# Performance work log

Measured on AMD Instinct MI355X. Metric: run time of the kernel, lower is better.

## Reference

```python
import jax, jax.numpy as jnp
import numpy as np

D_MODEL = 1024
NUM_HEADS = 16
D_K = D_MODEL // NUM_HEADS
D_FF = 4096


def setup_inputs() -> dict:
    key = jax.random.key(0)
    ks = jax.random.split(key, 12)
    s = 1.0 / np.sqrt(D_MODEL)
    sf = 1.0 / np.sqrt(D_FF)
    return {
        "x": jax.random.normal(ks[0], (2, 2048, D_MODEL), dtype=jnp.float32),
        # nn.Linear weights are [out_features, in_features]
        "Wq": jax.random.uniform(ks[1], (D_MODEL, D_MODEL), jnp.float32, -s, s),
        "Wk": jax.random.uniform(ks[2], (D_MODEL, D_MODEL), jnp.float32, -s, s),
        "Wv": jax.random.uniform(ks[3], (D_MODEL, D_MODEL), jnp.float32, -s, s),
        "Wo": jax.random.uniform(ks[4], (D_MODEL, D_MODEL), jnp.float32, -s, s),
        "W1": jax.random.uniform(ks[5], (D_FF, D_MODEL), jnp.float32, -s, s),
        "W2": jax.random.uniform(ks[6], (D_MODEL, D_FF), jnp.float32, -sf, sf),
        "g1": jnp.ones((D_MODEL,), jnp.float32),
        "b1": jnp.zeros((D_MODEL,), jnp.float32),
        "g2": jnp.ones((D_MODEL,), jnp.float32),
        "b2": jnp.zeros((D_MODEL,), jnp.float32),
    }


def _layer_norm(x, gamma, beta, eps=1e-5):
    mu = jnp.mean(x, axis=-1, keepdims=True)
    var = jnp.mean((x - mu) ** 2, axis=-1, keepdims=True)
    return (x - mu) * jax.lax.rsqrt(var + eps) * gamma + beta


def reference(x, Wq, Wk, Wv, Wo, W1, W2, g1, b1, g2, b2):
    B, S, _ = x.shape
    H, Dk = NUM_HEADS, D_K
    # projections (Linear: x @ W.T), split heads -> [B, H, S, Dk]
    q = (x @ Wq.T).reshape(B, S, H, Dk).transpose(0, 2, 1, 3)
    k = (x @ Wk.T).reshape(B, S, H, Dk).transpose(0, 2, 1, 3)
    v = (x @ Wv.T).reshape(B, S, H, Dk).transpose(0, 2, 1, 3)
    scores = jnp.einsum('bhsd,bhtd->bhst', q, k) / jnp.sqrt(jnp.float32(Dk))
    attn = jax.nn.softmax(scores, axis=-1)
    out = jnp.einsum('bhst,bhtd->bhsd', attn, v)
    out = out.transpose(0, 2, 1, 3).reshape(B, S, H * Dk)
    out = out @ Wo.T
    x_after_attn = _layer_norm(x + out, g1, b1)
    ff = jax.nn.gelu(x_after_attn @ W1.T, approximate=False)
    ff_out = ff @ W2.T
    return _layer_norm(x_after_attn + ff_out, g2, b2)
```

## Files before the change

### kernel.cpp

```cpp
#include <hip/hip_runtime.h>
#include <hip/hip_bf16.h>
#include <cstdint>
#include <cstddef>

#define D_MODEL 1024
#define D_FF    4096
#define NTOK    4096
#define SEQ     2048
#define NH      16
#define DK      64
#define LDQ     3072

typedef __bf16 bf16;
typedef __bf16 bf16_8 __attribute__((ext_vector_type(8)));
typedef __bf16 bf16_4 __attribute__((ext_vector_type(4)));
typedef float  f32_4  __attribute__((ext_vector_type(4)));

__device__ __forceinline__ void async_copy16(const bf16* g, bf16* l) {
    __builtin_amdgcn_global_load_lds((const __attribute__((address_space(1))) void*)g,
                                     (__attribute__((address_space(3))) void*)l,
                                     16, 0, 0);
}

__global__ __launch_bounds__(256)
void cast_all(const float* __restrict__ x,  const float* __restrict__ Wq,
              const float* __restrict__ Wk, const float* __restrict__ Wv,
              const float* __restrict__ Wo, const float* __restrict__ W1,
              const float* __restrict__ W2,
              bf16* __restrict__ xb, bf16* __restrict__ Wqkvb,
              bf16* __restrict__ Wob, bf16* __restrict__ W1b,
              bf16* __restrict__ W2b) {
    const int blk = blockIdx.x;
    const float* s; bf16* d; int off;
    if (blk < 4096)       { s = x;  d = xb;              off = blk; }
    else if (blk < 5120)  { s = Wq; d = Wqkvb;           off = blk - 4096; }
    else if (blk < 6144)  { s = Wk; d = Wqkvb + 1048576; off = blk - 5120; }
    else if (blk < 7168)  { s = Wv; d = Wqkvb + 2097152; off = blk - 6144; }
    else if (blk < 8192)  { s = Wo; d = Wob;             off = blk - 7168; }
    else if (blk < 12288) { s = W1; d = W1b;             off = blk - 8192; }
    else                  { s = W2; d = W2b;             off = blk - 12288; }
    const int i = off * 1024 + threadIdx.x * 4;
    float4 v = *(const float4*)(s + i);
    bf16_4 o;
    o[0] = (bf16)v.x; o[1] = (bf16)v.y; o[2] = (bf16)v.z; o[3] = (bf16)v.w;
    *(bf16_4*)(d + i) = o;
}

template <int EPI>
__global__ __launch_bounds__(256, 2)
void gemm_bt(const bf16* __restrict__ A, const bf16* __restrict__ B,
             bf16* __restrict__ C0, bf16* __restrict__ C1,
             int M, int N, int ldk, int kLen) {
    __shared__ bf16 As[128 * 32];
    __shared__ bf16 Bs[128 * 32];
    const int tid  = threadIdx.x;
    const int wave = tid >> 6, lane = tid & 63;
    const int quad = lane >> 4, l15 = lane & 15;
    const int wm = wave >> 1, wn = wave & 1;
    const int bm = blockIdx.x, bn = blockIdx.y, z = blockIdx.z;

    const bf16* A0 = A + (size_t)bm * 128 * ldk + (size_t)z * kLen;
    const bf16* B0 = B + (size_t)bn * 128 * ldk + (size_t)z * kLen;

    f32_4 acc[4][4];
#pragma unroll
    for (int i = 0; i < 4; i++)
#pragma unroll
        for (int j = 0; j < 4; j++) acc[i][j] = (f32_4){0.f, 0.f, 0.f, 0.f};

    const int ra = tid >> 2;
    const int gl = (tid & 3) ^ ((ra >> 1) & 3);
    const int ca = gl * 8;
    const int sx = (l15 >> 1) & 3;

    for (int k0 = 0; k0 < kLen; k0 += 32) {
#pragma unroll
        for (int c = 0; c < 2; c++)
            async_copy16(&A0[(size_t)(c * 64 + ra) * ldk + k0 + ca],
                         &As[c * 2048 + wave * 512]);
#pragma unroll
        for (int c = 0; c < 2; c++)
            async_copy16(&B0[(size_t)(c * 64 + ra) * ldk + k0 + ca],
                         &Bs[c * 2048 + wave * 512]);
        __syncthreads();

        bf16_8 af[4], bfr[4];
#pragma unroll
        for (int mi = 0; mi < 4; mi++)
            af[mi] = *(const bf16_8*)&As[(wm * 64 + mi * 16 + l15) * 32 + ((quad ^ sx) * 8)];
#pragma unroll
        for (int ni = 0; ni < 4; ni++)
            bfr[ni] = *(const bf16_8*)&Bs[(wn * 64 + ni * 16 + l15) * 32 + ((quad ^ sx) * 8)];
#pragma unroll
        for (int mi = 0; mi < 4; mi++)
#pragma unroll
            for (int ni = 0; ni < 4; ni++)
                acc[mi][ni] = __builtin_amdgcn_mfma_f32_16x16x32_bf16(
                    af[mi], bfr[ni], acc[mi][ni], 0, 0, 0);
        __syncthreads();
    }

    bf16* C = z ? C1 : C0;
    const int row0 = bm * 128 + wm * 64 + quad * 4;
    const int col0 = bn * 128 + wn * 64 + l15;
#pragma unroll
    for (int mi = 0; mi < 4; mi++) {
#pragma unroll
        for (int ni = 0; ni < 4; ni++) {
#pragma unroll
            for (int r = 0; r < 4; r++) {
                int row = row0 + mi * 16 + r;
                int col = col0 + ni * 16;
                size_t idx = (size_t)row * N + col;
                float v = acc[mi][ni][r];
                if (EPI == 0) {
                    C[idx] = (bf16)v;
                } else {
                    float g = 0.5f * v * (1.0f + erff(v * 0.70710678118654752f));
                    C[idx] = (bf16)g;
                }
            }
        }
    }
}

__global__ __launch_bounds__(256)
void transpose_v(const bf16* __restrict__ QKV, bf16* __restrict__ Vt) {
    __shared__ bf16 T[64 * 72];
    const int tb = blockIdx.x;
    const int cb = blockIdx.y;
    const int tid = threadIdx.x;
    const int r = tid >> 3, g = tid & 7;
#pragma unroll
    for (int c = 0; c < 2; ++c) {
        int row = c * 32 + r;
        bf16_8 v = *(const bf16_8*)&QKV[(size_t)(tb * 64 + row) * LDQ + 2048 + cb * 64 + g * 8];
        *(bf16_8*)&T[row * 72 + g * 8] = v;
    }
    __syncthreads();
    const int b  = (tb * 64) >> 11;
    const int s0 = (tb * 64) & 2047;
#pragma unroll
    for (int c = 0; c < 2; ++c) {
        int ch = c * 32 + r;
        bf16_8 v;
#pragma unroll
        for (int j = 0; j < 8; ++j) v[j] = T[(g * 8 + j) * 72 + ch];
        *(bf16_8*)&Vt[(size_t)(b * 1024 + cb * 64 + ch) * SEQ + s0 + g * 8] = v;
    }
}

__global__ __launch_bounds__(256)
void attn3(const bf16* __restrict__ QKV, const bf16* __restrict__ Vt,
           bf16* __restrict__ O) {
    __shared__ bf16 Ks[64 * 64];
    __shared__ bf16 Vs[64 * 64];
    __shared__ bf16 Ps[4][16 * 80];

    const int tid  = threadIdx.x;
    const int wave = tid >> 6, lane = tid & 63;
    const int quad = lane >> 4, l15 = lane & 15;
    const int qb = blockIdx.x & 31;
    const int h  = (blockIdx.x >> 5) & 15;
    const int b  = blockIdx.x >> 9;

    const bf16* Qg = QKV + (size_t)(b * SEQ) * LDQ + h * 64;
    const bf16* Kg = QKV + (size_t)(b * SEQ) * LDQ + 1024 + h * 64;
    const bf16* Vg = Vt + (size_t)(b * 1024 + h * 64) * SEQ;

    const int qrow = qb * 64 + wave * 16 + l15;
    const bf16_8 qf0 = *(const bf16_8*)&Qg[(size_t)qrow * LDQ + quad * 8];
    const bf16_8 qf1 = *(const bf16_8*)&Qg[(size_t)qrow * LDQ + 32 + quad * 8];

    const int srow = wave * 8 + (lane >> 3);
    const int sg   = lane & 7;
    const int xl   = l15 & 7;

    float l_lane = 0.f;
    f32_4 o_acc[4];
#pragma unroll
    for (int d = 0; d < 4; d++) o_acc[d] = (f32_4){0.f, 0.f, 0.f, 0.f};

    bf16* P = Ps[wave];

    for (int t = 0; t < SEQ / 64; ++t) {
        const int k0 = t * 64;
        __syncthreads();
#pragma unroll
        for (int c = 0; c < 2; ++c) {
            int r = c * 32 + srow;
            async_copy16(&Kg[(size_t)(k0 + r) * LDQ + ((sg ^ (r & 7)) * 8)],
                         &Ks[c * 2048 + wave * 512]);
            async_copy16(&Vg[(size_t)r * SEQ + k0 + ((sg ^ (r & 7)) * 8)],
                         &Vs[c * 2048 + wave * 512]);
        }
        __syncthreads();

        f32_4 s[4];
#pragma unroll
        for (int ni = 0; ni < 4; ni++) {
            const bf16* kp = &Ks[(ni * 16 + l15) * 64];
            bf16_8 kb0 = *(const bf16_8*)&kp[(quad ^ xl) * 8];
            bf16_8 kb1 = *(const bf16_8*)&kp[((quad + 4) ^ xl) * 8];
            f32_4 z = (f32_4){0.f, 0.f, 0.f, 0.f};
            s[ni] = __builtin_amdgcn_mfma_f32_16x16x32_bf16(kb0, qf0, z, 0, 0, 0);
            s[ni] = __builtin_amdgcn_mfma_f32_16x16x32_bf16(kb1, qf1, s[ni], 0, 0, 0);
        }

#pragma unroll
        for (int ni = 0; ni < 4; ni++) {
            bf16_4 pk;
#pragma unroll
            for (int r = 0; r < 4; r++) {
                float p = __expf(fmaf(s[ni][r], 0.125f, -8.0f));
                l_lane += p;
                pk[r] = (bf16)p;
            }
            int G = ni * 2 + (quad >> 1);
            *(bf16_4*)&P[l15 * 80 + ((G ^ xl) * 8) + ((quad & 1) * 4)] = pk;
        }
        bf16_8 pf0 = *(const bf16_8*)&P[l15 * 80 + ((quad ^ xl) * 8)];
        bf16_8 pf1 = *(const bf16_8*)&P[l15 * 80 + (((quad + 4) ^ xl) * 8)];

#pragma unroll
        for (int dt = 0; dt < 4; dt++) {
            const bf16* vp = &Vs[(dt * 16 + l15) * 64];
            bf16_8 vb0 = *(const bf16_8*)&vp[(quad ^ xl) * 8];
            bf16_8 vb1 = *(const bf16_8*)&vp[((quad + 4) ^ xl) * 8];
            o_acc[dt] = __builtin_amdgcn_mfma_f32_16x16x32_bf16(vb0, pf0, o_acc[dt], 0, 0, 0);
            o_acc[dt] = __builtin_amdgcn_mfma_f32_16x16x32_bf16(vb1, pf1, o_acc[dt], 0, 0, 0);
        }
    }

    l_lane += __shfl_xor(l_lane, 16);
    l_lane += __shfl_xor(l_lane, 32);
    const float rl = 1.0f / l_lane;

#pragma unroll
    for (int dt = 0; dt < 4; dt++) {
        bf16_4 pk;
#pragma unroll
        for (int r = 0; r < 4; r++) pk[r] = (bf16)(o_acc[dt][r] * rl);
        int G = dt * 2 + (quad >> 1);
        *(bf16_4*)&P[l15 * 80 + ((G ^ xl) * 8) + ((quad & 1) * 4)] = pk;
    }
    const int q2 = lane >> 2, dc = lane & 3, x2 = q2 & 7;
    bf16_8 o0 = *(const bf16_8*)&P[q2 * 80 + (((dc * 2) ^ x2) * 8)];
    bf16_8 o1 = *(const bf16_8*)&P[q2 * 80 + (((dc * 2 + 1) ^ x2) * 8)];
    const size_t row = (size_t)b * SEQ + qb * 64 + wave * 16 + q2;
    *(bf16_8*)&O[row * D_MODEL + h * 64 + dc * 16] = o0;
    *(bf16_8*)&O[row * D_MODEL + h * 64 + dc * 16 + 8] = o1;
}

template <bool A32, bool O32>
__global__ __launch_bounds__(256)
void ln_kernel(const void* __restrict__ av, const bf16* __restrict__ b0,
               const bf16* __restrict__ b1,
               const float* __restrict__ gamma, const float* __restrict__ beta,
               void* __restrict__ yv) {
    const int row = blockIdx.x;
    const int tid = threadIdx.x;
    const size_t off = (size_t)row * D_MODEL;
    float v[4];
    {
        bf16_4 p0 = *(const bf16_4*)(b0 + off + tid * 4);
        bf16_4 p1 = *(const bf16_4*)(b1 + off + tid * 4);
        if (A32) {
            float4 xa = *(const float4*)((const float*)av + off + tid * 4);
            v[0] = xa.x + (float)p0[0] + (float)p1[0];
            v[1] = xa.y + (float)p0[1] + (float)p1[1];
            v[2] = xa.z + (float)p0[2] + (float)p1[2];
            v[3] = xa.w + (float)p0[3] + (float)p1[3];
        } else {
            bf16_4 xa = *(const bf16_4*)((const bf16*)av + off + tid * 4);
#pragma unroll
            for (int i = 0; i < 4; i++)
                v[i] = (float)xa[i] + (float)p0[i] + (float)p1[i];
        }
    }
    float s = v[0] + v[1] + v[2] + v[3];
    float ss = v[0] * v[0] + v[1] * v[1] + v[2] * v[2] + v[3] * v[3];
#pragma unroll
    for (int m = 1; m < 64; m <<= 1) {
        s  += __shfl_xor(s, m);
        ss += __shfl_xor(ss, m);
    }
    __shared__ float red_s[4], red_q[4];
    int wave = tid >> 6, lane = tid & 63;
    if (lane == 0) { red_s[wave] = s; red_q[wave] = ss; }
    __syncthreads();
    s  = red_s[0] + red_s[1] + red_s[2] + red_s[3];
    ss = red_q[0] + red_q[1] + red_q[2] + red_q[3];
    float mu   = s * (1.f / D_MODEL);
    float var  = ss * (1.f / D_MODEL) - mu * mu;
    float rstd = rsqrtf(var + 1e-5f);
    float4 gg = *(const float4*)(gamma + tid * 4);
    float4 be = *(const float4*)(beta + tid * 4);
    float y0 = (v[0] - mu) * rstd * gg.x + be.x;
    float y1 = (v[1] - mu) * rstd * gg.y + be.y;
    float y2 = (v[2] - mu) * rstd * gg.z + be.z;
    float y3 = (v[3] - mu) * rstd * gg.w + be.w;
    if (O32) {
        *(float4*)((float*)yv + off + tid * 4) = make_float4(y0, y1, y2, y3);
    } else {
        bf16_4 o;
        o[0] = (bf16)y0; o[1] = (bf16)y1; o[2] = (bf16)y2; o[3] = (bf16)y3;
        *(bf16_4*)((bf16*)yv + off + tid * 4) = o;
    }
}

extern "C" void kernel_launch(void* const* d_in, const int* in_sizes, int n_in,
                              void* d_out, int out_size, void* d_ws, size_t ws_size,
                              hipStream_t stream) {
    (void)in_sizes; (void)n_in; (void)out_size; (void)ws_size;
    const float* x  = (const float*)d_in[0];
    const float* Wq = (const float*)d_in[1];
    const float* Wk = (const float*)d_in[2];
    const float* Wv = (const float*)d_in[3];
    const float* Wo = (const float*)d_in[4];
    const float* W1 = (const float*)d_in[5];
    const float* W2 = (const float*)d_in[6];
    const float* g1 = (const float*)d_in[7];
    const float* b1 = (const float*)d_in[8];
    const float* g2 = (const float*)d_in[9];
    const float* b2 = (const float*)d_in[10];

    char* ws = (char*)d_ws;
    bf16*  xb    = (bf16*)(ws + 0);
    bf16*  QKVb  = (bf16*)(ws + 8388608);
    bf16*  Vtb   = (bf16*)(ws + 33554432);
    bf16*  hb    = (bf16*)(ws + 8388608);
    bf16*  aob   = xb;
    bf16*  Wqkvb = (bf16*)(ws + 41943040);
    bf16*  Wob   = (bf16*)(ws + 48234496);
    bf16*  W1b   = (bf16*)(ws + 50331648);
    bf16*  W2b   = (bf16*)(ws + 58720256);
    bf16*  proj0 = (bf16*)(ws + 67108864);
    bf16*  proj1 = (bf16*)(ws + 75497472);
    bf16*  ln1b  = (bf16*)(ws + 83886080);

    cast_all<<<dim3(16384), 256, 0, stream>>>(x, Wq, Wk, Wv, Wo, W1, W2,
                                              xb, Wqkvb, Wob, W1b, W2b);

    gemm_bt<0><<<dim3(NTOK / 128, 3072 / 128, 1), 256, 0, stream>>>(
        xb, Wqkvb, QKVb, nullptr, NTOK, 3072, D_MODEL, D_MODEL);

    transpose_v<<<dim3(NTOK / 64, D_MODEL / 64), 256, 0, stream>>>(QKVb, Vtb);

    attn3<<<dim3(1024), 256, 0, stream>>>(QKVb, Vtb, aob);

    gemm_bt<0><<<dim3(NTOK / 128, D_MODEL / 128, 2), 256, 0, stream>>>(
        aob, Wob, proj0, proj1, NTOK, D_MODEL, D_MODEL, 512);
    ln_kernel<true, false><<<NTOK, 256, 0, stream>>>(x, proj0, proj1, g1, b1, ln1b);

    gemm_bt<2><<<dim3(NTOK / 128, D_FF / 128, 1), 256, 0, stream>>>(
        ln1b, W1b, hb, nullptr, NTOK, D_FF, D_MODEL, D_MODEL);

    gemm_bt<0><<<dim3(NTOK / 128, D_MODEL / 128, 2), 256, 0, stream>>>(
        hb, W2b, proj0, proj1, NTOK, D_MODEL, D_FF, 2048);
    ln_kernel<false, true><<<NTOK, 256, 0, stream>>>(ln1b, proj0, proj1, g2, b2, d_out);
}
```

Baseline: 346.5 us.

## Process two query groups per wave in attention and use 4-way split-K projections

After: 348.3 us. Within noise of the previous version (+0.5%).

```diff
diff --git a/kernel.cpp b/kernel.cpp
--- a/kernel.cpp
+++ b/kernel.cpp
@@ -49,7 +49,7 @@
 template <int EPI>
 __global__ __launch_bounds__(256, 2)
 void gemm_bt(const bf16* __restrict__ A, const bf16* __restrict__ B,
-             bf16* __restrict__ C0, bf16* __restrict__ C1,
+             bf16* __restrict__ C0, size_t cstride,
              int M, int N, int ldk, int kLen) {
     __shared__ bf16 As[128 * 32];
     __shared__ bf16 Bs[128 * 32];
@@ -100,7 +100,7 @@
         __syncthreads();
     }
 
-    bf16* C = z ? C1 : C0;
+    bf16* C = C0 + (size_t)z * cstride;
     const int row0 = bm * 128 + wm * 64 + quad * 4;
     const int col0 = bn * 128 + wn * 64 + l15;
 #pragma unroll
@@ -151,35 +151,41 @@
 }
 
 __global__ __launch_bounds__(256)
-void attn3(const bf16* __restrict__ QKV, const bf16* __restrict__ Vt,
+void attn4(const bf16* __restrict__ QKV, const bf16* __restrict__ Vt,
            bf16* __restrict__ O) {
     __shared__ bf16 Ks[64 * 64];
     __shared__ bf16 Vs[64 * 64];
-    __shared__ bf16 Ps[4][16 * 80];
+    __shared__ bf16 Ps[4][32 * 64];
 
     const int tid  = threadIdx.x;
     const int wave = tid >> 6, lane = tid & 63;
     const int quad = lane >> 4, l15 = lane & 15;
-    const int qb = blockIdx.x & 31;
-    const int h  = (blockIdx.x >> 5) & 15;
-    const int b  = blockIdx.x >> 9;
+    const int qb = blockIdx.x & 15;
+    const int h  = (blockIdx.x >> 4) & 15;
+    const int b  = blockIdx.x >> 8;
 
     const bf16* Qg = QKV + (size_t)(b * SEQ) * LDQ + h * 64;
     const bf16* Kg = QKV + (size_t)(b * SEQ) * LDQ + 1024 + h * 64;
     const bf16* Vg = Vt + (size_t)(b * 1024 + h * 64) * SEQ;
 
-    const int qrow = qb * 64 + wave * 16 + l15;
-    const bf16_8 qf0 = *(const bf16_8*)&Qg[(size_t)qrow * LDQ + quad * 8];
-    const bf16_8 qf1 = *(const bf16_8*)&Qg[(size_t)qrow * LDQ + 32 + quad * 8];
+    const int q0 = qb * 128 + wave * 32;
+    bf16_8 qf[2][2];
+#pragma unroll
+    for (int qg = 0; qg < 2; qg++)
+#pragma unroll
+        for (int j = 0; j < 2; j++)
+            qf[qg][j] = *(const bf16_8*)&Qg[(size_t)(q0 + qg * 16 + l15) * LDQ + j * 32 + quad * 8];
 
     const int srow = wave * 8 + (lane >> 3);
     const int sg   = lane & 7;
     const int xl   = l15 & 7;
 
-    float l_lane = 0.f;
-    f32_4 o_acc[4];
-#pragma unroll
-    for (int d = 0; d < 4; d++) o_acc[d] = (f32_4){0.f, 0.f, 0.f, 0.f};
+    float l_s[2] = {0.f, 0.f};
+    f32_4 o_acc[2][4];
+#pragma unroll
+    for (int qg = 0; qg < 2; qg++)
+#pragma unroll
+        for (int d = 0; d < 4; d++) o_acc[qg][d] = (f32_4){0.f, 0.f, 0.f, 0.f};
 
     bf16* P = Ps[wave];
 
@@ -196,66 +202,89 @@
         }
         __syncthreads();
 
-        f32_4 s[4];
+        f32_4 s[2][4];
 #pragma unroll
         for (int ni = 0; ni < 4; ni++) {
             const bf16* kp = &Ks[(ni * 16 + l15) * 64];
             bf16_8 kb0 = *(const bf16_8*)&kp[(quad ^ xl) * 8];
             bf16_8 kb1 = *(const bf16_8*)&kp[((quad + 4) ^ xl) * 8];
-            f32_4 z = (f32_4){0.f, 0.f, 0.f, 0.f};
-            s[ni] = __builtin_amdgcn_mfma_f32_16x16x32_bf16(kb0, qf0, z, 0, 0, 0);
-            s[ni] = __builtin_amdgcn_mfma_f32_16x16x32_bf16(kb1, qf1, s[ni], 0, 0, 0);
-        }
-
-#pragma unroll
-        for (int ni = 0; ni < 4; ni++) {
-            bf16_4 pk;
-#pragma unroll
-            for (int r = 0; r < 4; r++) {
-                float p = __expf(fmaf(s[ni][r], 0.125f, -8.0f));
-                l_lane += p;
-                pk[r] = (bf16)p;
+#pragma unroll
+            for (int qg = 0; qg < 2; qg++) {
+                f32_4 z = (f32_4){0.f, 0.f, 0.f, 0.f};
+                z = __builtin_amdgcn_mfma_f32_16x16x32_bf16(kb0, qf[qg][0], z, 0, 0, 0);
+                s[qg][ni] = __builtin_amdgcn_mfma_f32_16x16x32_bf16(kb1, qf[qg][1], z, 0, 0, 0);
             }
-            int G = ni * 2 + (quad >> 1);
-            *(bf16_4*)&P[l15 * 80 + ((G ^ xl) * 8) + ((quad & 1) * 4)] = pk;
-        }
-        bf16_8 pf0 = *(const bf16_8*)&P[l15 * 80 + ((quad ^ xl) * 8)];
-        bf16_8 pf1 = *(const bf16_8*)&P[l15 * 80 + (((quad + 4) ^ xl) * 8)];
+        }
+
+#pragma unroll
+        for (int qg = 0; qg < 2; qg++)
+#pragma unroll
+            for (int ni = 0; ni < 4; ni++) {
+                bf16_4 pk;
+#pragma unroll
+                for (int r = 0; r < 4; r++) {
+                    float p = exp2f(fmaf(s[qg][ni][r], 0.18033688011112042f,
+                                         -11.541560327111707f));
+                    l_s[qg] += p;
+                    pk[r] = (bf16)p;
+                }
+                int G = ni * 2 + (quad >> 1);
+                *(bf16_4*)&P[(qg * 16 + l15) * 64 + ((G ^ xl) * 8) + ((quad & 1) * 4)] = pk;
+            }
+        bf16_8 pf[2][2];
+#pragma unroll
+        for (int qg = 0; qg < 2; qg++) {
+            pf[qg][0] = *(const bf16_8*)&P[(qg * 16 + l15) * 64 + ((quad ^ xl) * 8)];
+            pf[qg][1] = *(const bf16_8*)&P[(qg * 16 + l15) * 64 + (((quad + 4) ^ xl) * 8)];
+        }
 
 #pragma unroll
         for (int dt = 0; dt < 4; dt++) {
             const bf16* vp = &Vs[(dt * 16 + l15) * 64];
             bf16_8 vb0 = *(const bf16_8*)&vp[(quad ^ xl) * 8];
             bf16_8 vb1 = *(const bf16_8*)&vp[((quad + 4) ^ xl) * 8];
-            o_acc[dt] = __builtin_amdgcn_mfma_f32_16x16x32_bf16(vb0, pf0, o_acc[dt], 0, 0, 0);
-            o_acc[dt] = __builtin_amdgcn_mfma_f32_16x16x32_bf16(vb1, pf1, o_acc[dt], 0, 0, 0);
-        }
-    }
-
-    l_lane += __shfl_xor(l_lane, 16);
-    l_lane += __shfl_xor(l_lane, 32);
-    const float rl = 1.0f / l_lane;
-
-#pragma unroll
-    for (int dt = 0; dt < 4; dt++) {
-        bf16_4 pk;
-#pragma unroll
-        for (int r = 0; r < 4; r++) pk[r] = (bf16)(o_acc[dt][r] * rl);
-        int G = dt * 2 + (quad >> 1);
-        *(bf16_4*)&P[l15 * 80 + ((G ^ xl) * 8) + ((quad & 1) * 4)] = pk;
-    }
-    const int q2 = lane >> 2, dc = lane & 3, x2 = q2 & 7;
-    bf16_8 o0 = *(const bf16_8*)&P[q2 * 80 + (((dc * 2) ^ x2) * 8)];
-    bf16_8 o1 = *(const bf16_8*)&P[q2 * 80 + (((dc * 2 + 1) ^ x2) * 8)];
-    const size_t row = (size_t)b * SEQ + qb * 64 + wave * 16 + q2;
-    *(bf16_8*)&O[row * D_MODEL + h * 64 + dc * 16] = o0;
-    *(bf16_8*)&O[row * D_MODEL + h * 64 + dc * 16 + 8] = o1;
+#pragma unroll
+            for (int qg = 0; qg < 2; qg++) {
+                o_acc[qg][dt] = __builtin_amdgcn_mfma_f32_16x16x32_bf16(
+                    vb0, pf[qg][0], o_acc[qg][dt], 0, 0, 0);
+                o_acc[qg][dt] = __builtin_amdgcn_mfma_f32_16x16x32_bf16(
+                    vb1, pf[qg][1], o_acc[qg][dt], 0, 0, 0);
+            }
+        }
+    }
+
+#pragma unroll
+    for (int qg = 0; qg < 2; qg++) {
+        l_s[qg] += __shfl_xor(l_s[qg], 16);
+        l_s[qg] += __shfl_xor(l_s[qg], 32);
+        l_s[qg] = 1.0f / l_s[qg];
+    }
+
+#pragma unroll
+    for (int qg = 0; qg < 2; qg++)
+#pragma unroll
+        for (int dt = 0; dt < 4; dt++) {
+            bf16_4 pk;
+#pragma unroll
+            for (int r = 0; r < 4; r++) pk[r] = (bf16)(o_acc[qg][dt][r] * l_s[qg]);
+            int G = dt * 2 + (quad >> 1);
+            *(bf16_4*)&P[(qg * 16 + l15) * 64 + ((G ^ xl) * 8) + ((quad & 1) * 4)] = pk;
+        }
+#pragma unroll
+    for (int pass = 0; pass < 4; pass++) {
+        int rowl = pass * 8 + (lane >> 3);
+        int g = lane & 7;
+        bf16_8 ov = *(const bf16_8*)&P[rowl * 64 + ((g ^ (rowl & 7)) * 8)];
+        size_t grow = (size_t)b * SEQ + qb * 128 + wave * 32 + rowl;
+        *(bf16_8*)&O[grow * D_MODEL + h * 64 + g * 8] = ov;
+    }
 }
 
 template <bool A32, bool O32>
 __global__ __launch_bounds__(256)
-void ln_kernel(const void* __restrict__ av, const bf16* __restrict__ b0,
-               const bf16* __restrict__ b1,
+void ln_kernel(const void* __restrict__ av, const bf16* __restrict__ p0,
+               const bf16* __restrict__ p1, const bf16* __restrict__ p2,
+               const bf16* __restrict__ p3,
                const float* __restrict__ gamma, const float* __restrict__ beta,
                void* __restrict__ yv) {
     const int row = blockIdx.x;
@@ -263,20 +292,21 @@
     const size_t off = (size_t)row * D_MODEL;
     float v[4];
     {
-        bf16_4 p0 = *(const bf16_4*)(b0 + off + tid * 4);
-        bf16_4 p1 = *(const bf16_4*)(b1 + off + tid * 4);
+        bf16_4 a0 = *(const bf16_4*)(p0 + off + tid * 4);
+        bf16_4 a1 = *(const bf16_4*)(p1 + off + tid * 4);
+        bf16_4 a2 = *(const bf16_4*)(p2 + off + tid * 4);
+        bf16_4 a3 = *(const bf16_4*)(p3 + off + tid * 4);
         if (A32) {
             float4 xa = *(const float4*)((const float*)av + off + tid * 4);
-            v[0] = xa.x + (float)p0[0] + (float)p1[0];
-            v[1] = xa.y + (float)p0[1] + (float)p1[1];
-            v[2] = xa.z + (float)p0[2] + (float)p1[2];
-            v[3] = xa.w + (float)p0[3] + (float)p1[3];
+            v[0] = xa.x; v[1] = xa.y; v[2] = xa.z; v[3] = xa.w;
         } else {
             bf16_4 xa = *(const bf16_4*)((const bf16*)av + off + tid * 4);
 #pragma unroll
-            for (int i = 0; i < 4; i++)
-                v[i] = (float)xa[i] + (float)p0[i] + (float)p1[i];
-        }
+            for (int i = 0; i < 4; i++) v[i] = (float)xa[i];
+        }
+#pragma unroll
+        for (int i = 0; i < 4; i++)
+            v[i] += ((float)a0[i] + (float)a1[i]) + ((float)a2[i] + (float)a3[i]);
     }
     float s = v[0] + v[1] + v[2] + v[3];
     float ss = v[0] * v[0] + v[1] * v[1] + v[2] * v[2] + v[3] * v[3];
@@ -327,36 +357,40 @@
 
     char* ws = (char*)d_ws;
     bf16*  xb    = (bf16*)(ws + 0);
+    bf16*  aob   = xb;
+    bf16*  ln1b  = (bf16*)(ws + 0);
     bf16*  QKVb  = (bf16*)(ws + 8388608);
     bf16*  Vtb   = (bf16*)(ws + 33554432);
     bf16*  hb    = (bf16*)(ws + 8388608);
-    bf16*  aob   = xb;
     bf16*  Wqkvb = (bf16*)(ws + 41943040);
     bf16*  Wob   = (bf16*)(ws + 48234496);
     bf16*  W1b   = (bf16*)(ws + 50331648);
     bf16*  W2b   = (bf16*)(ws + 58720256);
     bf16*  proj0 = (bf16*)(ws + 67108864);
-    bf16*  proj1 = (bf16*)(ws + 75497472);
-    bf16*  ln1b  = (bf16*)(ws + 83886080);
+    const size_t PSTRIDE = (size_t)NTOK * D_MODEL;
 
     cast_all<<<dim3(16384), 256, 0, stream>>>(x, Wq, Wk, Wv, Wo, W1, W2,
                                               xb, Wqkvb, Wob, W1b, W2b);
 
     gemm_bt<0><<<dim3(NTOK / 128, 3072 / 128, 1), 256, 0, stream>>>(
-        xb, Wqkvb, QKVb, nullptr, NTOK, 3072, D_MODEL, D_MODEL);
+        xb, Wqkvb, QKVb, 0, NTOK, 3072, D_MODEL, D_MODEL);
 
     transpose_v<<<dim3(NTOK / 64, D_MODEL / 64), 256, 0, stream>>>(QKVb, Vtb);
 
-    attn3<<<dim3(1024), 256, 0, stream>>>(QKVb, Vtb, aob);
-
-    gemm_bt<0><<<dim3(NTOK / 128, D_MODEL / 128, 2), 256, 0, stream>>>(
-        aob, Wob, proj0, proj1, NTOK, D_MODEL, D_MODEL, 512);
-    ln_kernel<true, false><<<NTOK, 256, 0, stream>>>(x, proj0, proj1, g1, b1, ln1b);
+    attn4<<<dim3(512), 256, 0, stream>>>(QKVb, Vtb, aob);
+
+    gemm_bt<0><<<dim3(NTOK / 128, D_MODEL / 128, 4), 256, 0, stream>>>(
+        aob, Wob, proj0, PSTRIDE, NTOK, D_MODEL, D_MODEL, 256);
+    ln_kernel<true, false><<<NTOK, 256, 0, stream>>>(
+        x, proj0, proj0 + PSTRIDE, proj0 + 2 * PSTRIDE, proj0 + 3 * PSTRIDE,
+        g1, b1, ln1b);
 
     gemm_bt<2><<<dim3(NTOK / 128, D_FF / 128, 1), 256, 0, stream>>>(
-        ln1b, W1b, hb, nullptr, NTOK, D_FF, D_MODEL, D_MODEL);
-
-    gemm_bt<0><<<dim3(NTOK / 128, D_MODEL / 128, 2), 256, 0, stream>>>(
-        hb, W2b, proj0, proj1, NTOK, D_MODEL, D_FF, 2048);
-    ln_kernel<false, true><<<NTOK, 256, 0, stream>>>(ln1b, proj0, proj1, g2, b2, d_out);
-}
+        ln1b, W1b, hb, 0, NTOK, D_FF, D_MODEL, D_MODEL);
+
+    gemm_bt<0><<<dim3(NTOK / 128, D_MODEL / 128, 4), 256, 0, stream>>>(
+        hb, W2b, proj0, PSTRIDE, NTOK, D_MODEL, D_FF, 1024);
+    ln_kernel<false, true><<<NTOK, 256, 0, stream>>>(
+        ln1b, proj0, proj0 + PSTRIDE, proj0 + 2 * PSTRIDE, proj0 + 3 * PSTRIDE,
+        g2, b2, d_out);
+}
```

## Fuse V transpose into QKV GEMM epilogue and use four-way split-K projections

Applied to the files above, without the earlier changes.

Measured after the change: 346.8 us. About the same (+0.1%).

```diff
diff --git a/kernel.cpp b/kernel.cpp
--- a/kernel.cpp
+++ b/kernel.cpp
@@ -49,7 +49,7 @@
 template <int EPI>
 __global__ __launch_bounds__(256, 2)
 void gemm_bt(const bf16* __restrict__ A, const bf16* __restrict__ B,
-             bf16* __restrict__ C0, bf16* __restrict__ C1,
+             bf16* __restrict__ C0, size_t cstride, bf16* __restrict__ Vt,
              int M, int N, int ldk, int kLen) {
     __shared__ bf16 As[128 * 32];
     __shared__ bf16 Bs[128 * 32];
@@ -100,9 +100,27 @@
         __syncthreads();
     }
 
-    bf16* C = z ? C1 : C0;
+    bf16* C = C0 + (size_t)z * cstride;
     const int row0 = bm * 128 + wm * 64 + quad * 4;
     const int col0 = bn * 128 + wn * 64 + l15;
+
+    if (EPI == 3 && bn >= 16) {
+        const int bvt  = bm >> 4;
+#pragma unroll
+        for (int mi = 0; mi < 4; mi++) {
+            const int srow = (row0 + mi * 16) & 2047;
+#pragma unroll
+            for (int ni = 0; ni < 4; ni++) {
+                const int ch = col0 + ni * 16 - 2048;
+                bf16_4 w;
+#pragma unroll
+                for (int r = 0; r < 4; r++) w[r] = (bf16)acc[mi][ni][r];
+                *(bf16_4*)&Vt[((size_t)(bvt * 1024 + ch)) * SEQ + srow] = w;
+            }
+        }
+        return;
+    }
+
 #pragma unroll
     for (int mi = 0; mi < 4; mi++) {
 #pragma unroll
@@ -113,40 +131,14 @@
                 int col = col0 + ni * 16;
                 size_t idx = (size_t)row * N + col;
                 float v = acc[mi][ni][r];
-                if (EPI == 0) {
-                    C[idx] = (bf16)v;
-                } else {
+                if (EPI == 2) {
                     float g = 0.5f * v * (1.0f + erff(v * 0.70710678118654752f));
                     C[idx] = (bf16)g;
+                } else {
+                    C[idx] = (bf16)v;
                 }
             }
         }
-    }
-}
-
-__global__ __launch_bounds__(256)
-void transpose_v(const bf16* __restrict__ QKV, bf16* __restrict__ Vt) {
-    __shared__ bf16 T[64 * 72];
-    const int tb = blockIdx.x;
-    const int cb = blockIdx.y;
-    const int tid = threadIdx.x;
-    const int r = tid >> 3, g = tid & 7;
-#pragma unroll
-    for (int c = 0; c < 2; ++c) {
-        int row = c * 32 + r;
-        bf16_8 v = *(const bf16_8*)&QKV[(size_t)(tb * 64 + row) * LDQ + 2048 + cb * 64 + g * 8];
-        *(bf16_8*)&T[row * 72 + g * 8] = v;
-    }
-    __syncthreads();
-    const int b  = (tb * 64) >> 11;
-    const int s0 = (tb * 64) & 2047;
-#pragma unroll
-    for (int c = 0; c < 2; ++c) {
-        int ch = c * 32 + r;
-        bf16_8 v;
-#pragma unroll
-        for (int j = 0; j < 8; ++j) v[j] = T[(g * 8 + j) * 72 + ch];
-        *(bf16_8*)&Vt[(size_t)(b * 1024 + cb * 64 + ch) * SEQ + s0 + g * 8] = v;
     }
 }
 
@@ -203,8 +195,8 @@
             bf16_8 kb0 = *(const bf16_8*)&kp[(quad ^ xl) * 8];
             bf16_8 kb1 = *(const bf16_8*)&kp[((quad + 4) ^ xl) * 8];
             f32_4 z = (f32_4){0.f, 0.f, 0.f, 0.f};
-            s[ni] = __builtin_amdgcn_mfma_f32_16x16x32_bf16(kb0, qf0, z, 0, 0, 0);
-            s[ni] = __builtin_amdgcn_mfma_f32_16x16x32_bf16(kb1, qf1, s[ni], 0, 0, 0);
+            z = __builtin_amdgcn_mfma_f32_16x16x32_bf16(kb0, qf0, z, 0, 0, 0);
+            s[ni] = __builtin_amdgcn_mfma_f32_16x16x32_bf16(kb1, qf1, z, 0, 0, 0);
         }
 
 #pragma unroll
@@ -212,7 +204,8 @@
             bf16_4 pk;
 #pragma unroll
             for (int r = 0; r < 4; r++) {
-                float p = __expf(fmaf(s[ni][r], 0.125f, -8.0f));
+                float p = exp2f(fmaf(s[ni][r], 0.18033688011112042f,
+                                     -11.541560327111707f));
                 l_lane += p;
                 pk[r] = (bf16)p;
             }
@@ -254,8 +247,9 @@
 
 template <bool A32, bool O32>
 __global__ __launch_bounds__(256)
-void ln_kernel(const void* __restrict__ av, const bf16* __restrict__ b0,
-               const bf16* __restrict__ b1,
+void ln_kernel(const void* __restrict__ av, const bf16* __restrict__ p0,
+               const bf16* __restrict__ p1, const bf16* __restrict__ p2,
+               const bf16* __restrict__ p3,
                const float* __restrict__ gamma, const float* __restrict__ beta,
                void* __restrict__ yv) {
     const int row = blockIdx.x;
@@ -263,20 +257,21 @@
     const size_t off = (size_t)row * D_MODEL;
     float v[4];
     {
-        bf16_4 p0 = *(const bf16_4*)(b0 + off + tid * 4);
-        bf16_4 p1 = *(const bf16_4*)(b1 + off + tid * 4);
+        bf16_4 a0 = *(const bf16_4*)(p0 + off + tid * 4);
+        bf16_4 a1 = *(const bf16_4*)(p1 + off + tid * 4);
+        bf16_4 a2 = *(const bf16_4*)(p2 + off + tid * 4);
+        bf16_4 a3 = *(const bf16_4*)(p3 + off + tid * 4);
         if (A32) {
             float4 xa = *(const float4*)((const float*)av + off + tid * 4);
-            v[0] = xa.x + (float)p0[0] + (float)p1[0];
-            v[1] = xa.y + (float)p0[1] + (float)p1[1];
-            v[2] = xa.z + (float)p0[2] + (float)p1[2];
-            v[3] = xa.w + (float)p0[3] + (float)p1[3];
+            v[0] = xa.x; v[1] = xa.y; v[2] = xa.z; v[3] = xa.w;
         } else {
             bf16_4 xa = *(const bf16_4*)((const bf16*)av + off + tid * 4);
 #pragma unroll
-            for (int i = 0; i < 4; i++)
-                v[i] = (float)xa[i] + (float)p0[i] + (float)p1[i];
-        }
+            for (int i = 0; i < 4; i++) v[i] = (float)xa[i];
+        }
+#pragma unroll
+        for (int i = 0; i < 4; i++)
+            v[i] += ((float)a0[i] + (float)a1[i]) + ((float)a2[i] + (float)a3[i]);
     }
     float s = v[0] + v[1] + v[2] + v[3];
     float ss = v[0] * v[0] + v[1] * v[1] + v[2] * v[2] + v[3] * v[3];
@@ -327,36 +322,38 @@
 
     char* ws = (char*)d_ws;
     bf16*  xb    = (bf16*)(ws + 0);
+    bf16*  aob   = xb;
+    bf16*  ln1b  = (bf16*)(ws + 0);
     bf16*  QKVb  = (bf16*)(ws + 8388608);
     bf16*  Vtb   = (bf16*)(ws + 33554432);
     bf16*  hb    = (bf16*)(ws + 8388608);
-    bf16*  aob   = xb;
     bf16*  Wqkvb = (bf16*)(ws + 41943040);
     bf16*  Wob   = (bf16*)(ws + 48234496);
     bf16*  W1b   = (bf16*)(ws + 50331648);
     bf16*  W2b   = (bf16*)(ws + 58720256);
     bf16*  proj0 = (bf16*)(ws + 67108864);
-    bf16*  proj1 = (bf16*)(ws + 75497472);
-    bf16*  ln1b  = (bf16*)(ws + 83886080);
+    const size_t PSTRIDE = (size_t)NTOK * D_MODEL;
 
     cast_all<<<dim3(16384), 256, 0, stream>>>(x, Wq, Wk, Wv, Wo, W1, W2,
                                               xb, Wqkvb, Wob, W1b, W2b);
 
-    gemm_bt<0><<<dim3(NTOK / 128, 3072 / 128, 1), 256, 0, stream>>>(
-        xb, Wqkvb, QKVb, nullptr, NTOK, 3072, D_MODEL, D_MODEL);
-
-    transpose_v<<<dim3(NTOK / 64, D_MODEL / 64), 256, 0, stream>>>(QKVb, Vtb);
+    gemm_bt<3><<<dim3(NTOK / 128, 3072 / 128, 1), 256, 0, stream>>>(
+        xb, Wqkvb, QKVb, 0, Vtb, NTOK, 3072, D_MODEL, D_MODEL);
 
     attn3<<<dim3(1024), 256, 0, stream>>>(QKVb, Vtb, aob);
 
-    gemm_bt<0><<<dim3(NTOK / 128, D_MODEL / 128, 2), 256, 0, stream>>>(
-        aob, Wob, proj0, proj1, NTOK, D_MODEL, D_MODEL, 512);
-    ln_kernel<true, false><<<NTOK, 256, 0, stream>>>(x, proj0, proj1, g1, b1, ln1b);
+    gemm_bt<0><<<dim3(NTOK / 128, D_MODEL / 128, 4), 256, 0, stream>>>(
+        aob, Wob, proj0, PSTRIDE, nullptr, NTOK, D_MODEL, D_MODEL, 256);
+    ln_kernel<true, false><<<NTOK, 256, 0, stream>>>(
+        x, proj0, proj0 + PSTRIDE, proj0 + 2 * PSTRIDE, proj0 + 3 * PSTRIDE,
+        g1, b1, ln1b);
 
     gemm_bt<2><<<dim3(NTOK / 128, D_FF / 128, 1), 256, 0, stream>>>(
-        ln1b, W1b, hb, nullptr, NTOK, D_FF, D_MODEL, D_MODEL);
-
-    gemm_bt<0><<<dim3(NTOK / 128, D_MODEL / 128, 2), 256, 0, stream>>>(
-        hb, W2b, proj0, proj1, NTOK, D_MODEL, D_FF, 2048);
-    ln_kernel<false, true><<<NTOK, 256, 0, stream>>>(ln1b, proj0, proj1, g2, b2, d_out);
-}
+        ln1b, W1b, hb, 0, nullptr, NTOK, D_FF, D_MODEL, D_MODEL);
+
+    gemm_bt<0><<<dim3(NTOK / 128, D_MODEL / 128, 4), 256, 0, stream>>>(
+        hb, W2b, proj0, PSTRIDE, nullptr, NTOK, D_MODEL, D_FF, 1024);
+    ln_kernel<false, true><<<NTOK, 256, 0, stream>>>(
+        ln1b, proj0, proj0 + PSTRIDE, proj0 + 2 * PSTRIDE, proj0 + 3 * PSTRIDE,
+        g2, b2, d_out);
+}
```
